# Performance work log

Hardware: AMD Instinct MI355X
Metric: run time of the kernel (lower is better)

Reference implementation:

```python
import jax, jax.numpy as jnp
import numpy as np

NU = 0.01 / np.pi  # viscosity buffer from the torch module


def _mlp(x, W_in, b_in, W_hid, b_hid, W_out, b_out):
    # x: [N, 2] -> u: [N, 1]; tanh MLP with stacked hidden layers scanned.
    h = jnp.tanh(x @ W_in + b_in)

    def step(h, wb):
        W, b = wb
        return jnp.tanh(h @ W + b), None

    h, _ = jax.lax.scan(step, h, (W_hid, b_hid))
    return h @ W_out + b_out


def setup_inputs() -> dict:
    key = jax.random.key(0)
    ks = jax.random.split(key, 10)
    N_f, N0, Nb, H, L = 131072, 4096, 2048, 128, 7
    s_in = 1.0 / np.sqrt(2.0)
    s_h = 1.0 / np.sqrt(H)
    return {
        "x_f": jax.random.normal(ks[0], (N_f, 2), jnp.float32),
        "x0_cat": jax.random.normal(ks[1], (N0, 2), jnp.float32),
        "xb_left_cat": jax.random.normal(ks[2], (Nb, 2), jnp.float32),
        "xb_right_cat": jax.random.normal(ks[3], (Nb, 2), jnp.float32),
        "W_in": jax.random.normal(ks[4], (2, H), jnp.float32) * s_in,
        "b_in": jax.random.normal(ks[5], (H,), jnp.float32) * 0.01,
        "W_hid": jax.random.normal(ks[6], (L, H, H), jnp.float32) * s_h,
        "b_hid": jax.random.normal(ks[7], (L, H), jnp.float32) * 0.01,
        "W_out": jax.random.normal(ks[8], (H, 1), jnp.float32) * s_h,
        "b_out": jax.random.normal(ks[9], (1,), jnp.float32) * 0.01,
    }


def reference(x_f, x0_cat, xb_left_cat, xb_right_cat,
              W_in, b_in, W_hid, b_hid, W_out, b_out):
    u = lambda x: _mlp(x, W_in, b_in, W_hid, b_hid, W_out, b_out)

    u_0_pred = u(x0_cat)
    u_b_left_pred = u(xb_left_cat)
    u_b_right_pred = u(xb_right_cat)

    u_f_pred = u(x_f)  # [N_f, 1]

    # Each row of u depends only on the matching row of x, so grad of the sum
    # yields per-example gradients (equivalent to torch.autograd.grad with
    # grad_outputs=ones).
    usum = lambda x: u(x).sum()
    g = jax.grad(usum)(x_f)            # [N_f, 2]
    u_x = g[:, 0:1]
    u_t = g[:, 1:2]

    # Second derivative: grad of sum(u_x) w.r.t. x, take the x-component.
    uxx_full = jax.grad(lambda x: jax.grad(usum)(x)[:, 0].sum())(x_f)
    u_xx = uxx_full[:, 0:1]

    pde_residual = u_t + u_f_pred * u_x - NU * u_xx
    return jnp.concatenate((u_0_pred, u_b_left_pred, u_b_right_pred,
                            pde_residual), axis=0)
```

## Files before the change

kernel.cpp:

```cpp
#include <hip/hip_runtime.h>
#include <math.h>

#define NU_F 0.0031830988618379067f
#define KTANH 2.885390082f

typedef _Float16 f16x8  __attribute__((ext_vector_type(8)));
typedef float    f32x4  __attribute__((ext_vector_type(4)));
typedef float    f32x16 __attribute__((ext_vector_type(16)));

__device__ __forceinline__ float tanh_pre(float zs) {
    float e = __builtin_amdgcn_exp2f(zs);
    float r = __builtin_amdgcn_rcpf(e + 1.0f);
    return fmaf(-2.0f, r, 1.0f);
}

__device__ __forceinline__ unsigned pkf16(float a, float b) {
    auto v = __builtin_amdgcn_cvt_pkrtz(a, b);
    return __builtin_bit_cast(unsigned, v);
}

__global__ void prep_wfrag(const float* __restrict__ Whid, _Float16* __restrict__ wcf)
{
    const int t    = blockIdx.x * 256 + threadIdx.x;
    const int lane = t & 63;
    const int f    = t >> 6;
    const int ks = f & 7;
    const int nt = (f >> 3) & 3;
    const int l  = f >> 5;
    const int n  = lane & 31;
    const int hi = lane >> 5;
    const int ch = ((nt >> 1) << 6) + n * 2 + (nt & 1);
    const int kk = ks * 16 + hi * 8;
    const float* src = Whid + l * 16384 + kk * 128 + ch;
    f16x8 v;
    #pragma unroll
    for (int jj = 0; jj < 8; ++jj)
        v[jj] = (_Float16)src[jj * 128];
    *(f16x8*)(wcf + (size_t)t * 8) = v;
}

#define RS 68
#define MFMA32(A, B, C) __builtin_amdgcn_mfma_f32_32x32x16_f16((A), (B), (C), 0, 0, 0)

__global__ __launch_bounds__(256, 4)
void pinn_fused(const float* __restrict__ xf,
                const float* __restrict__ x0,  const float* __restrict__ xbl,
                const float* __restrict__ xbr,
                const float* __restrict__ Win,  const float* __restrict__ bin,
                const float* __restrict__ bhid,
                const float* __restrict__ Wout, const float* __restrict__ bout,
                const _Float16* __restrict__ wcf,
                float* __restrict__ out)
{
    __shared__ unsigned Hh[2][64 * RS];
    __shared__ float xpt[128];
    __shared__ float pbuf[256];
    __shared__ float dots[64];

    const int tid  = threadIdx.x;
    const int lane = tid & 63;
    const int wv   = tid >> 6;
    const int nl   = lane & 31;
    const int hi   = lane >> 5;
    const int mt   = wv & 1;
    const int ntp  = wv >> 1;
    const int cdw  = ntp * 32 + nl;
    const int blk  = blockIdx.x;
    const bool isv = (blk >= 8192);

    if (!isv) {
        if (tid < 32) xpt[tid] = xf[blk * 32 + tid];
    } else {
        if (tid < 128) {
            const int vb = blk - 8192;
            const float* src = (vb < 64) ? (x0 + vb * 128)
                             : (vb < 96) ? (xbl + (vb - 64) * 128)
                                         : (xbr + (vb - 96) * 128);
            xpt[tid] = src[tid];
        }
    }
    __syncthreads();

    const int cp = tid & 63;
    {
        const float2 w01 = *(const float2*)&Win[cp * 2];
        const float2 w11 = *(const float2*)&Win[128 + cp * 2];
        const float2 bb  = *(const float2*)&bin[cp * 2];
        const float w01sx = w01.x * KTANH, w01sy = w01.y * KTANH;
        const float w11sx = w11.x * KTANH, w11sy = w11.y * KTANH;
        const float bbsx  = bb.x  * KTANH, bbsy  = bb.y  * KTANH;
        if (!isv) {
            const int p0 = wv * 4;
            #pragma unroll
            for (int i = 0; i < 4; ++i) {
                const int p = p0 + i;
                const float x = xpt[2 * p], tt = xpt[2 * p + 1];
                const float ya = tanh_pre(fmaf(x, w01sx, fmaf(tt, w11sx, bbsx)));
                const float yb = tanh_pre(fmaf(x, w01sy, fmaf(tt, w11sy, bbsy)));
                const float da = 1.f - ya * ya, db = 1.f - yb * yb;
                Hh[0][(p * 4 + 0) * RS + cp] = pkf16(ya, yb);
                Hh[0][(p * 4 + 1) * RS + cp] = pkf16(da * w01.x, db * w01.y);
                Hh[0][(p * 4 + 2) * RS + cp] = pkf16(da * w11.x, db * w11.y);
                Hh[0][(p * 4 + 3) * RS + cp] =
                    pkf16(-2.f * ya * da * w01.x * w01.x,
                          -2.f * yb * db * w01.y * w01.y);
            }
        } else {
            const int p0 = wv * 16;
            #pragma unroll
            for (int i = 0; i < 16; ++i) {
                const int p = p0 + i;
                const float x = xpt[2 * p], tt = xpt[2 * p + 1];
                const float ya = tanh_pre(fmaf(x, w01sx, fmaf(tt, w11sx, bbsx)));
                const float yb = tanh_pre(fmaf(x, w01sy, fmaf(tt, w11sy, bbsy)));
                Hh[0][p * RS + cp] = pkf16(ya, yb);
            }
        }
    }
    __syncthreads();

    const _Float16* pb0 = wcf + ntp * 8192 + lane * 8;
    const _Float16* pb1 = pb0 + 4096;
    const int arow = (mt * 32 + nl) * RS + hi * 4;

    if (!isv) {
        for (int l = 0; l < 7; ++l) {
            const unsigned* Hc = Hh[l & 1];
            unsigned*       Hn = Hh[(l & 1) ^ 1];
            const float2 bt = *(const float2*)&bhid[l * 128 + ntp * 64 + nl * 2];
            const float bbs0 = bt.x * KTANH, bbs1 = bt.y * KTANH;

            f32x16 a0, a1;
            #pragma unroll
            for (int i = 0; i < 16; ++i) { a0[i] = 0.f; a1[i] = 0.f; }

            #pragma unroll
            for (int ks = 0; ks < 8; ++ks) {
                const f16x8 A  = *(const f16x8*)&Hc[arow + ks * 8];
                const f16x8 B0 = *(const f16x8*)(pb0 + ks * 512);
                const f16x8 B1 = *(const f16x8*)(pb1 + ks * 512);
                a0 = MFMA32(A, B0, a0);
                a1 = MFMA32(A, B1, a1);
            }

            #pragma unroll
            for (int q = 0; q < 4; ++q) {
                float h0[4], h1[4];
                {
                    const float zx = a0[q * 4 + 1], zt = a0[q * 4 + 2],
                                zxx = a0[q * 4 + 3];
                    const float y = tanh_pre(fmaf(a0[q * 4 + 0], KTANH, bbs0));
                    const float d = fmaf(-y, y, 1.f);
                    const float m = d * zx;
                    h0[0] = y; h0[1] = m; h0[2] = d * zt;
                    h0[3] = fmaf(d, zxx, -2.f * (y * m) * zx);
                }
                {
                    const float zx = a1[q * 4 + 1], zt = a1[q * 4 + 2],
                                zxx = a1[q * 4 + 3];
                    const float y = tanh_pre(fmaf(a1[q * 4 + 0], KTANH, bbs1));
                    const float d = fmaf(-y, y, 1.f);
                    const float m = d * zx;
                    h1[0] = y; h1[1] = m; h1[2] = d * zt;
                    h1[3] = fmaf(d, zxx, -2.f * (y * m) * zx);
                }
                const int rbase = mt * 32 + q * 8 + hi * 4;
                #pragma unroll
                for (int s = 0; s < 4; ++s)
                    Hn[(rbase + s) * RS + cdw] = pkf16(h0[s], h1[s]);
            }
            pb0 += 16384; pb1 += 16384;
            __syncthreads();
        }
    } else {
        for (int l = 0; l < 7; ++l) {
            const unsigned* Hc = Hh[l & 1];
            unsigned*       Hn = Hh[(l & 1) ^ 1];
            const float2 bt = *(const float2*)&bhid[l * 128 + ntp * 64 + nl * 2];
            const float bbs0 = bt.x * KTANH, bbs1 = bt.y * KTANH;

            f32x16 a0, a1;
            #pragma unroll
            for (int i = 0; i < 16; ++i) { a0[i] = 0.f; a1[i] = 0.f; }

            #pragma unroll
            for (int ks = 0; ks < 8; ++ks) {
                const f16x8 A  = *(const f16x8*)&Hc[arow + ks * 8];
                const f16x8 B0 = *(const f16x8*)(pb0 + ks * 512);
                const f16x8 B1 = *(const f16x8*)(pb1 + ks * 512);
                a0 = MFMA32(A, B0, a0);
                a1 = MFMA32(A, B1, a1);
            }

            #pragma unroll
            for (int r = 0; r < 16; ++r) {
                const float y0 = tanh_pre(fmaf(a0[r], KTANH, bbs0));
                const float y1 = tanh_pre(fmaf(a1[r], KTANH, bbs1));
                const int row = mt * 32 + (r & 3) + (r >> 2) * 8 + hi * 4;
                Hn[row * RS + cdw] = pkf16(y0, y1);
            }
            pb0 += 16384; pb1 += 16384;
            __syncthreads();
        }
    }

    {
        const int st = lane;
        const int cb = wv * 16;
        float part = 0.f;
        #pragma unroll
        for (int c8 = 0; c8 < 4; ++c8) {
            const f16x8 hv = *(const f16x8*)&Hh[1][st * RS + cb + c8 * 4];
            const float4 w1 = *(const float4*)&Wout[wv * 32 + c8 * 8];
            const float4 w2 = *(const float4*)&Wout[wv * 32 + c8 * 8 + 4];
            part = fmaf((float)hv[0], w1.x, part);
            part = fmaf((float)hv[1], w1.y, part);
            part = fmaf((float)hv[2], w1.z, part);
            part = fmaf((float)hv[3], w1.w, part);
            part = fmaf((float)hv[4], w2.x, part);
            part = fmaf((float)hv[5], w2.y, part);
            part = fmaf((float)hv[6], w2.z, part);
            part = fmaf((float)hv[7], w2.w, part);
        }
        pbuf[wv * 64 + st] = part;
    }
    __syncthreads();
    if (tid < 64) {
        const float sum = (pbuf[tid] + pbuf[64 + tid])
                        + (pbuf[128 + tid] + pbuf[192 + tid]);
        const int d = isv ? tid : ((tid & 3) * 16 + (tid >> 2));
        dots[d] = sum;
    }
    __syncthreads();
    if (!isv) {
        if (tid < 16) {
            const float u = dots[tid] + bout[0];
            out[8192 + blk * 16 + tid] =
                dots[32 + tid] + u * dots[16 + tid] - NU_F * dots[48 + tid];
        }
    } else {
        if (tid < 64) out[(blk - 8192) * 64 + tid] = dots[tid] + bout[0];
    }
}

extern "C" void kernel_launch(void* const* d_in, const int* in_sizes, int n_in,
                              void* d_out, int out_size, void* d_ws, size_t ws_size,
                              hipStream_t stream) {
    (void)in_sizes; (void)n_in; (void)ws_size; (void)out_size;
    const float* xf   = (const float*)d_in[0];
    const float* x0   = (const float*)d_in[1];
    const float* xbl  = (const float*)d_in[2];
    const float* xbr  = (const float*)d_in[3];
    const float* Win  = (const float*)d_in[4];
    const float* bin  = (const float*)d_in[5];
    const float* Whid = (const float*)d_in[6];
    const float* bhid = (const float*)d_in[7];
    const float* Wout = (const float*)d_in[8];
    const float* bout = (const float*)d_in[9];
    float* out = (float*)d_out;

    _Float16* wcf = (_Float16*)d_ws;

    hipLaunchKernelGGL(prep_wfrag, dim3(14336 / 256), dim3(256), 0, stream,
                       Whid, wcf);
    hipLaunchKernelGGL(pinn_fused, dim3(8192 + 128), dim3(256), 0, stream,
                       xf, x0, xbl, xbr, Win, bin, bhid, Wout, bout, wcf, out);
}
```

Measured before the change: 245.1 us.

## Prefetch next-layer weight fragments into registers and use LDS-only barriers

Each layer's weight B fragments and bias now go into registers, and the next layer's fragments are fetched from global memory right after the current MFMA loop, so the load overlaps the tanh epilogue and LDS writes. __syncthreads is replaced by a barrier that waits only on LDS counters, so in-flight global prefetches are not drained at each layer boundary. This adds about 16 f16x8 registers per thread, which may lower occupancy. It also relies on the global loads not being needed before the barrier.

```diff
diff --git a/kernel.cpp b/kernel.cpp
--- a/kernel.cpp
+++ b/kernel.cpp
@@ -17,6 +17,11 @@
 __device__ __forceinline__ unsigned pkf16(float a, float b) {
     auto v = __builtin_amdgcn_cvt_pkrtz(a, b);
     return __builtin_bit_cast(unsigned, v);
+}
+
+__device__ __forceinline__ void lds_barrier() {
+    asm volatile("s_waitcnt lgkmcnt(0)" ::: "memory");
+    __builtin_amdgcn_s_barrier();
 }
 
 __global__ void prep_wfrag(const float* __restrict__ Whid, _Float16* __restrict__ wcf)
@@ -79,6 +84,17 @@
             xpt[tid] = src[tid];
         }
     }
+
+    const _Float16* pb = wcf + ntp * 8192 + lane * 8;
+    const float* bptr = bhid + ntp * 64 + nl * 2;
+    f16x8 B0[8], B1[8];
+    #pragma unroll
+    for (int ks = 0; ks < 8; ++ks) {
+        B0[ks] = *(const f16x8*)(pb + ks * 512);
+        B1[ks] = *(const f16x8*)(pb + 4096 + ks * 512);
+    }
+    float2 btc = *(const float2*)bptr;
+
     __syncthreads();
 
     const int cp = tid & 63;
@@ -117,18 +133,15 @@
             }
         }
     }
-    __syncthreads();
-
-    const _Float16* pb0 = wcf + ntp * 8192 + lane * 8;
-    const _Float16* pb1 = pb0 + 4096;
+    lds_barrier();
+
     const int arow = (mt * 32 + nl) * RS + hi * 4;
 
     if (!isv) {
         for (int l = 0; l < 7; ++l) {
             const unsigned* Hc = Hh[l & 1];
             unsigned*       Hn = Hh[(l & 1) ^ 1];
-            const float2 bt = *(const float2*)&bhid[l * 128 + ntp * 64 + nl * 2];
-            const float bbs0 = bt.x * KTANH, bbs1 = bt.y * KTANH;
+            const float bbs0 = btc.x * KTANH, bbs1 = btc.y * KTANH;
 
             f32x16 a0, a1;
             #pragma unroll
@@ -136,11 +149,20 @@
 
             #pragma unroll
             for (int ks = 0; ks < 8; ++ks) {
-                const f16x8 A  = *(const f16x8*)&Hc[arow + ks * 8];
-                const f16x8 B0 = *(const f16x8*)(pb0 + ks * 512);
-                const f16x8 B1 = *(const f16x8*)(pb1 + ks * 512);
-                a0 = MFMA32(A, B0, a0);
-                a1 = MFMA32(A, B1, a1);
+                const f16x8 A = *(const f16x8*)&Hc[arow + ks * 8];
+                a0 = MFMA32(A, B0[ks], a0);
+                a1 = MFMA32(A, B1[ks], a1);
+            }
+
+            pb += 16384;
+            if (l < 6) {
+                #pragma unroll
+                for (int ks = 0; ks < 8; ++ks) {
+                    B0[ks] = *(const f16x8*)(pb + ks * 512);
+                    B1[ks] = *(const f16x8*)(pb + 4096 + ks * 512);
+                }
+                btc = *(const float2*)(bptr + 128);
+                bptr += 128;
             }
 
             #pragma unroll
@@ -169,15 +191,13 @@
                 for (int s = 0; s < 4; ++s)
                     Hn[(rbase + s) * RS + cdw] = pkf16(h0[s], h1[s]);
             }
-            pb0 += 16384; pb1 += 16384;
-            __syncthreads();
+            lds_barrier();
         }
     } else {
         for (int l = 0; l < 7; ++l) {
             const unsigned* Hc = Hh[l & 1];
             unsigned*       Hn = Hh[(l & 1) ^ 1];
-            const float2 bt = *(const float2*)&bhid[l * 128 + ntp * 64 + nl * 2];
-            const float bbs0 = bt.x * KTANH, bbs1 = bt.y * KTANH;
+            const float bbs0 = btc.x * KTANH, bbs1 = btc.y * KTANH;
 
             f32x16 a0, a1;
             #pragma unroll
@@ -185,11 +205,20 @@
 
             #pragma unroll
             for (int ks = 0; ks < 8; ++ks) {
-                const f16x8 A  = *(const f16x8*)&Hc[arow + ks * 8];
-                const f16x8 B0 = *(const f16x8*)(pb0 + ks * 512);
-                const f16x8 B1 = *(const f16x8*)(pb1 + ks * 512);
-                a0 = MFMA32(A, B0, a0);
-                a1 = MFMA32(A, B1, a1);
+                const f16x8 A = *(const f16x8*)&Hc[arow + ks * 8];
+                a0 = MFMA32(A, B0[ks], a0);
+                a1 = MFMA32(A, B1[ks], a1);
+            }
+
+            pb += 16384;
+            if (l < 6) {
+                #pragma unroll
+                for (int ks = 0; ks < 8; ++ks) {
+                    B0[ks] = *(const f16x8*)(pb + ks * 512);
+                    B1[ks] = *(const f16x8*)(pb + 4096 + ks * 512);
+                }
+                btc = *(const float2*)(bptr + 128);
+                bptr += 128;
             }
 
             #pragma unroll
@@ -199,8 +228,7 @@
                 const int row = mt * 32 + (r & 3) + (r >> 2) * 8 + hi * 4;
                 Hn[row * RS + cdw] = pkf16(y0, y1);
             }
-            pb0 += 16384; pb1 += 16384;
-            __syncthreads();
+            lds_barrier();
         }
     }
 
@@ -224,14 +252,14 @@
         }
         pbuf[wv * 64 + st] = part;
     }
-    __syncthreads();
+    lds_barrier();
     if (tid < 64) {
         const float sum = (pbuf[tid] + pbuf[64 + tid])
                         + (pbuf[128 + tid] + pbuf[192 + tid]);
         const int d = isv ? tid : ((tid & 3) * 16 + (tid >> 2));
         dots[d] = sum;
     }
-    __syncthreads();
+    lds_barrier();
     if (!isv) {
         if (tid < 16) {
             const float u = dots[tid] + bout[0];
```

Measured after the change: 331.6 us. 1.35x slower.
